# Kernel optimization log

Measured on AMD Instinct MI355X. Metric: run time of the kernel, lower is better.

The kernel has to match this reference:

```python
import jax, jax.numpy as jnp
import numpy as np

V, D, F, H, L = 32000, 1024, 4096, 16, 6
HD = D // H
EPS = 1e-5


def _posenc(S):
    pos = jnp.arange(S, dtype=jnp.float32)[:, None]
    div = jnp.exp(jnp.arange(0, D, 2, dtype=jnp.float32) * (-jnp.log(10000.0) / D))
    enc = jnp.zeros((S, D), jnp.float32)
    enc = enc.at[:, 0::2].set(jnp.sin(pos * div))
    enc = enc.at[:, 1::2].set(jnp.cos(pos * div))
    return enc


def _mha(xq, xkv, Wq, bq, Wk, bk, Wv, bv, Wo, bo, causal):
    B, Sq, _ = xq.shape
    Sk = xkv.shape[1]
    q = (xq @ Wq.T + bq).reshape(B, Sq, H, HD)
    k = (xkv @ Wk.T + bk).reshape(B, Sk, H, HD)
    v = (xkv @ Wv.T + bv).reshape(B, Sk, H, HD)
    scores = jnp.einsum('bqhd,bkhd->bhqk', q, k) / jnp.sqrt(jnp.float32(HD))
    if causal:
        mask = jnp.tril(jnp.ones((Sq, Sk), dtype=bool))
        scores = jnp.where(mask, scores, -jnp.inf)
    w = jax.nn.softmax(scores, axis=-1)
    out = jnp.einsum('bhqk,bkhd->bqhd', w, v).reshape(B, Sq, D)
    return out @ Wo.T + bo


def _ln(x, g, b):
    mu = jnp.mean(x, axis=-1, keepdims=True)
    var = jnp.mean((x - mu) ** 2, axis=-1, keepdims=True)
    return (x - mu) / jnp.sqrt(var + EPS) * g + b


def setup_inputs() -> dict:
    key = jax.random.key(0)
    ks = jax.random.split(key, 32)
    B, S, Se = 4, 512, 512
    s = 0.02
    inp = {
        'text': jax.random.randint(ks[0], (B, S), 0, V),
        'encoder_output': jax.random.normal(ks[1], (B, Se, D), jnp.float32),
        'W_e': jax.random.normal(ks[2], (V, D), jnp.float32) * s,
        'b_out': jnp.zeros((V,), jnp.float32),
        'ln_g': jnp.ones((D,), jnp.float32),
        'ln_b': jnp.zeros((D,), jnp.float32),
        'W1': jax.random.normal(ks[3], (F, D), jnp.float32) * s,
        'b1': jnp.zeros((F,), jnp.float32),
        'W2': jax.random.normal(ks[4], (D, F), jnp.float32) * s,
        'b2': jnp.zeros((D,), jnp.float32),
    }
    names = ['mWq', 'mWk', 'mWv', 'mWo', 'cWq', 'cWk', 'cWv', 'cWo']
    for i, n in enumerate(names):
        inp[n] = jax.random.normal(ks[5 + i], (D, D), jnp.float32) * s
        inp[n.replace('W', 'b')] = jnp.zeros((D,), jnp.float32)
    return inp


def reference(text, encoder_output, W_e, b_out, ln_g, ln_b, W1, b1, W2, b2,
              mWq, mbq, mWk, mbk, mWv, mbv, mWo, mbo,
              cWq, cbq, cWk, cbk, cWv, cbv, cWo, cbo):
    # embed + sinusoidal positional encoding (dropout is identity in eval)
    x = W_e[text] + _posenc(text.shape[1])[None, :, :]
    # NOTE: the torch module reuses the SAME attention/FFN/LN weights each layer
    for _ in range(L):
        a = _ln(x + _mha(x, x, mWq, mbq, mWk, mbk, mWv, mbv, mWo, mbo, True), ln_g, ln_b)
        c = _ln(_mha(a, encoder_output, cWq, cbq, cWk, cbk, cWv, cbv, cWo, cbo, False) + a, ln_g, ln_b)
        f = jax.nn.relu(c @ W1.T + b1) @ W2.T + b2
        x = _ln(c + f, ln_g, ln_b)
    logits = x @ W_e.T + b_out  # tied embedding weights
    # nn.Softmax() with dim=None on a 3-D tensor -> torch legacy dim=0
    return jax.nn.softmax(logits, axis=0)
```

## Files before the change

### kernel.cpp

```cpp
#include <hip/hip_runtime.h>

#define D_MODEL 1024
#define SEQ     512
#define NBATCH  4
#define NHEAD   16
#define HDIM    64
#define NTOK    2048
#define VOCAB   32000
#define FFDIM   4096
#define VCHUNK  6400
#define MiB     (1024*1024)

typedef _Float16 f16;
typedef f16   f16x8 __attribute__((ext_vector_type(8)));
typedef float f32x4 __attribute__((ext_vector_type(4)));

__device__ __forceinline__ void async_cp16(f16* lds, const f16* g) {
    __builtin_amdgcn_global_load_lds(
        (const __attribute__((address_space(1))) unsigned int*)g,
        (__attribute__((address_space(3))) unsigned int*)lds, 16, 0, 0);
}

__device__ __forceinline__ float block_sum(float v, float* lds) {
    #pragma unroll
    for (int o = 1; o < 64; o <<= 1) v += __shfl_xor(v, o);
    int w = threadIdx.x >> 6;
    if ((threadIdx.x & 63) == 0) lds[w] = v;
    __syncthreads();
    v = lds[0] + lds[1] + lds[2] + lds[3];
    __syncthreads();
    return v;
}
__device__ __forceinline__ float block_max(float v, float* lds) {
    #pragma unroll
    for (int o = 1; o < 64; o <<= 1) v = fmaxf(v, __shfl_xor(v, o));
    int w = threadIdx.x >> 6;
    if ((threadIdx.x & 63) == 0) lds[w] = v;
    __syncthreads();
    v = fmaxf(fmaxf(lds[0], lds[1]), fmaxf(lds[2], lds[3]));
    __syncthreads();
    return v;
}

__global__ __launch_bounds__(256) void f32_to_f16_kernel(
    const float* __restrict__ in, f16* __restrict__ out, int n)
{
    int i0 = blockIdx.x * 1024 + threadIdx.x;
    #pragma unroll
    for (int e = 0; e < 4; e++) {
        int i = i0 + e * 256;
        if (i < n) out[i] = (f16)in[i];
    }
}

__global__ __launch_bounds__(256) void embed_kernel(
    const int* __restrict__ text, const float* __restrict__ We,
    float* __restrict__ X, f16* __restrict__ X16)
{
    int t = blockIdx.x;
    int s = t & (SEQ - 1);
    int tok = text[t];
    int tid = threadIdx.x;
    const float kf = 9.210340371976184f / 1024.f;
    #pragma unroll
    for (int e = 0; e < 4; e++) {
        int d = tid + e * 256;
        int i2 = d & ~1;
        float freq = expf(-(float)i2 * kf);
        float ang = (float)s * freq;
        float pe = (d & 1) ? cosf(ang) : sinf(ang);
        float v = We[(size_t)tok * D_MODEL + d] + pe;
        X[(size_t)t * D_MODEL + d] = v;
        X16[(size_t)t * D_MODEL + d] = (f16)v;
    }
}

template<bool RELU, int OUTMODE, int BM, bool QKV3>
__global__ __launch_bounds__(256) void gemm16_kernel(
    const f16* __restrict__ A, const f16* __restrict__ W,
    const float* __restrict__ bias, const float* __restrict__ bias2,
    const float* __restrict__ bias3,
    float* __restrict__ C, f16* __restrict__ C16, int M, int N, int K)
{
    constexpr int AM = BM / 2;
    constexpr int TM = AM / 16;
    __shared__ __align__(16) f16 As[BM * 32];
    __shared__ __align__(16) f16 Bs[128 * 32];
    const int tid  = threadIdx.x;
    const int lane = tid & 63;
    const int wv   = tid >> 6;
    const int wr   = (wv >> 1) * AM;
    const int wc   = (wv & 1) * 64;
    const int m0 = blockIdx.y * BM;
    const int n0 = blockIdx.x * 128;
    const int lm = lane & 15;
    const int lk = (lane >> 4) * 8;

    f32x4 acc[TM][4] = {};

    for (int k0 = 0; k0 < K; k0 += 32) {
        #pragma unroll
        for (int e = 0; e < BM / 64; e++) {
            int s = tid + e * 256;
            int row = s >> 2, cb = s & 3;
            async_cp16(&As[s * 8], &A[(size_t)(m0 + row) * K + k0 + cb * 8]);
        }
        #pragma unroll
        for (int e = 0; e < 2; e++) {
            int s = tid + e * 256;
            int row = s >> 2, cb = s & 3;
            async_cp16(&Bs[s * 8], &W[(size_t)(n0 + row) * K + k0 + cb * 8]);
        }
        __syncthreads();
        f16x8 af[TM], bfr[4];
        #pragma unroll
        for (int i = 0; i < TM; i++)
            af[i]  = *(const f16x8*)&As[(wr + i * 16 + lm) * 32 + lk];
        #pragma unroll
        for (int j = 0; j < 4; j++)
            bfr[j] = *(const f16x8*)&Bs[(wc + j * 16 + lm) * 32 + lk];
        #pragma unroll
        for (int i = 0; i < TM; i++)
            #pragma unroll
            for (int j = 0; j < 4; j++)
                acc[i][j] = __builtin_amdgcn_mfma_f32_16x16x32_f16(
                    af[i], bfr[j], acc[i][j], 0, 0, 0);
        __syncthreads();
    }

    const int rq = (lane >> 4) * 4;
    #pragma unroll
    for (int i = 0; i < TM; i++) {
        #pragma unroll
        for (int j = 0; j < 4; j++) {
            int col = n0 + wc + j * 16 + lm;
            float bj;
            if (QKV3) {
                const float* bp = col < 1024 ? bias : (col < 2048 ? bias2 : bias3);
                bj = bp[col & 1023];
            } else {
                bj = bias[col];
            }
            #pragma unroll
            for (int r = 0; r < 4; r++) {
                int row = m0 + wr + i * 16 + rq + r;
                float v = acc[i][j][r] + bj;
                if (RELU) v = fmaxf(v, 0.f);
                if (OUTMODE == 0) C[(size_t)row * N + col] = v;
                else              C16[(size_t)row * N + col] = (f16)v;
            }
        }
    }
}

template<int CAUSAL>
__global__ __launch_bounds__(256) void attn_scores16_kernel(
    const f16* __restrict__ Qb, const f16* __restrict__ Kb,
    float* __restrict__ Sc, int ldq, int ldk, int qoff, int koff)
{
    const int bh = blockIdx.z;
    const int b = bh >> 4, h = bh & 15;
    const int q0 = blockIdx.y * 128, k0 = blockIdx.x * 128;
    const int tid = threadIdx.x;
    float* out = Sc + (size_t)bh * SEQ * SEQ;

    if (CAUSAL && k0 >= q0 + 128) {
        const f32x4 mv = {-1e30f, -1e30f, -1e30f, -1e30f};
        #pragma unroll
        for (int e = 0; e < 16; e++) {
            int idx = tid + e * 256;
            int rr = idx >> 5, c4 = (idx & 31) * 4;
            *(f32x4*)&out[(size_t)(q0 + rr) * SEQ + k0 + c4] = mv;
        }
        return;
    }

    __shared__ __align__(16) f16 As[128 * 64];
    __shared__ __align__(16) f16 Bs[128 * 64];
    const f16* Qg = Qb + (size_t)(b * SEQ + q0) * ldq + qoff + h * HDIM;
    const f16* Kg = Kb + (size_t)(b * SEQ + k0) * ldk + koff + h * HDIM;
    #pragma unroll
    for (int e = 0; e < 4; e++) {
        int s = tid + e * 256;
        int ks = s >> 9, row = (s >> 2) & 127, cb = s & 3;
        async_cp16(&As[s * 8], &Qg[(size_t)row * ldq + ks * 32 + cb * 8]);
        async_cp16(&Bs[s * 8], &Kg[(size_t)row * ldk + ks * 32 + cb * 8]);
    }
    __syncthreads();

    const int lane = tid & 63;
    const int wv   = tid >> 6;
    const int wr   = (wv >> 1) * 64;
    const int wc   = (wv & 1) * 64;
    const int lm   = lane & 15;
    const int lk   = (lane >> 4) * 8;
    f32x4 acc[4][4] = {};
    #pragma unroll
    for (int ks = 0; ks < 2; ks++) {
        f16x8 af[4], bf[4];
        #pragma unroll
        for (int i = 0; i < 4; i++)
            af[i] = *(const f16x8*)&As[ks * 4096 + (wr + i * 16 + lm) * 32 + lk];
        #pragma unroll
        for (int j = 0; j < 4; j++)
            bf[j] = *(const f16x8*)&Bs[ks * 4096 + (wc + j * 16 + lm) * 32 + lk];
        #pragma unroll
        for (int i = 0; i < 4; i++)
            #pragma unroll
            for (int j = 0; j < 4; j++)
                acc[i][j] = __builtin_amdgcn_mfma_f32_16x16x32_f16(
                    af[i], bf[j], acc[i][j], 0, 0, 0);
    }

    const int rq = (lane >> 4) * 4;
    #pragma unroll
    for (int i = 0; i < 4; i++)
        #pragma unroll
        for (int j = 0; j < 4; j++)
            #pragma unroll
            for (int r = 0; r < 4; r++) {
                int qq = q0 + wr + i * 16 + rq + r;
                int kk = k0 + wc + j * 16 + lm;
                float v = acc[i][j][r] * 0.125f;
                if (CAUSAL && kk > qq) v = -1e30f;
                out[(size_t)qq * SEQ + kk] = v;
            }
}

__global__ __launch_bounds__(256) void softmax_row_kernel(
    const float* __restrict__ Sc, f16* __restrict__ P)
{
    __shared__ float lds[4];
    size_t row = blockIdx.x;
    const float* p = Sc + row * SEQ;
    int tid = threadIdx.x;
    float v0 = p[tid], v1 = p[tid + 256];
    float m = block_max(fmaxf(v0, v1), lds);
    float e0 = expf(v0 - m), e1 = expf(v1 - m);
    float s = block_sum(e0 + e1, lds);
    float inv = 1.f / s;
    f16* q = P + row * SEQ;
    q[tid]       = (f16)(e0 * inv);
    q[tid + 256] = (f16)(e1 * inv);
}

__global__ __launch_bounds__(256) void attn_av16_kernel(
    const f16* __restrict__ P, const f16* __restrict__ Vt,
    f16* __restrict__ O16)
{
    __shared__ __align__(16) f16 Ps[64 * 32];
    __shared__ __align__(16) f16 Vs[64 * 32];
    const int bh = blockIdx.y;
    const int b = bh >> 4, h = bh & 15;
    const int q0 = blockIdx.x * 64;
    const int tid  = threadIdx.x;
    const int lane = tid & 63;
    const int wv   = tid >> 6;
    const int wr   = (wv >> 1) * 32;
    const int wc   = (wv & 1) * 32;
    const int lm   = lane & 15;
    const int lk   = (lane >> 4) * 8;
    const f16* Pg = P  + ((size_t)bh * SEQ + q0) * SEQ;
    const f16* Vg = Vt + (size_t)bh * HDIM * SEQ;

    f32x4 acc[2][2] = {};
    for (int k0 = 0; k0 < SEQ; k0 += 32) {
        int row = tid >> 2, cb = tid & 3;
        async_cp16(&Ps[tid * 8], &Pg[(size_t)row * SEQ + k0 + cb * 8]);
        async_cp16(&Vs[tid * 8], &Vg[(size_t)row * SEQ + k0 + cb * 8]);
        __syncthreads();
        f16x8 af[2], bf[2];
        #pragma unroll
        for (int i = 0; i < 2; i++)
            af[i] = *(const f16x8*)&Ps[(wr + i * 16 + lm) * 32 + lk];
        #pragma unroll
        for (int j = 0; j < 2; j++)
            bf[j] = *(const f16x8*)&Vs[(wc + j * 16 + lm) * 32 + lk];
        #pragma unroll
        for (int i = 0; i < 2; i++)
            #pragma unroll
            for (int j = 0; j < 2; j++)
                acc[i][j] = __builtin_amdgcn_mfma_f32_16x16x32_f16(
                    af[i], bf[j], acc[i][j], 0, 0, 0);
        __syncthreads();
    }

    const int rq = (lane >> 4) * 4;
    #pragma unroll
    for (int i = 0; i < 2; i++)
        #pragma unroll
        for (int j = 0; j < 2; j++)
            #pragma unroll
            for (int r = 0; r < 4; r++)
                O16[(size_t)(b * SEQ + q0 + wr + i * 16 + rq + r) * D_MODEL
                    + h * HDIM + wc + j * 16 + lm] = (f16)acc[i][j][r];
}

__global__ __launch_bounds__(256) void vtrans_kernel(
    const f16* __restrict__ V, f16* __restrict__ Vt, int ldv, int vbase)
{
    __shared__ __align__(16) f16 t[64][72];
    const int bh = blockIdx.y;
    const int b = bh >> 4, h = bh & 15;
    const int s0 = blockIdx.x * 64;
    const int tid = threadIdx.x;
    const int r = tid >> 3;
    const int c8 = (tid & 7) * 8;
    #pragma unroll
    for (int half = 0; half < 2; half++) {
        int row = r + half * 32;
        f16x8 v = *(const f16x8*)&V[(size_t)(b * SEQ + s0 + row) * ldv
                                    + vbase + h * HDIM + c8];
        #pragma unroll
        for (int j = 0; j < 8; j++) t[c8 + j][row] = v[j];
    }
    __syncthreads();
    const int d = tid >> 2;
    const int sblk = (tid & 3) * 16;
    f16* dst = Vt + ((size_t)bh * HDIM + d) * SEQ + s0 + sblk;
    *(f16x8*)&dst[0] = *(const f16x8*)&t[d][sblk];
    *(f16x8*)&dst[8] = *(const f16x8*)&t[d][sblk + 8];
}

__global__ __launch_bounds__(256) void add_ln_kernel(
    const float* __restrict__ X, const float* __restrict__ Y,
    const float* __restrict__ g, const float* __restrict__ bb,
    float* __restrict__ Out, f16* __restrict__ Out16)
{
    __shared__ float lds[4];
    int row = blockIdx.x;
    const float* xp = X + (size_t)row * D_MODEL;
    const float* yp = Y + (size_t)row * D_MODEL;
    int tid = threadIdx.x;
    float s[4];
    float lsum = 0.f;
    #pragma unroll
    for (int e = 0; e < 4; e++) {
        int d = tid + e * 256;
        s[e] = xp[d] + yp[d];
        lsum += s[e];
    }
    float mu = block_sum(lsum, lds) * (1.f / D_MODEL);
    float lv = 0.f;
    #pragma unroll
    for (int e = 0; e < 4; e++) { float t = s[e] - mu; lv += t * t; }
    float rstd = rsqrtf(block_sum(lv, lds) * (1.f / D_MODEL) + 1e-5f);
    #pragma unroll
    for (int e = 0; e < 4; e++) {
        int d = tid + e * 256;
        float v = (s[e] - mu) * rstd * g[d] + bb[d];
        Out[(size_t)row * D_MODEL + d] = v;
        Out16[(size_t)row * D_MODEL + d] = (f16)v;
    }
}

__global__ __launch_bounds__(256) void softmax_axis0_chunk_kernel(
    const float* __restrict__ L, float* __restrict__ out, int cv0)
{
    int idx = blockIdx.x * 256 + threadIdx.x;
    if (idx >= SEQ * VCHUNK) return;
    int s = idx / VCHUNK;
    int c = idx - s * VCHUNK;
    float v0 = L[((size_t)(0 * SEQ + s)) * VCHUNK + c];
    float v1 = L[((size_t)(1 * SEQ + s)) * VCHUNK + c];
    float v2 = L[((size_t)(2 * SEQ + s)) * VCHUNK + c];
    float v3 = L[((size_t)(3 * SEQ + s)) * VCHUNK + c];
    float m = fmaxf(fmaxf(v0, v1), fmaxf(v2, v3));
    float e0 = expf(v0 - m), e1 = expf(v1 - m), e2 = expf(v2 - m), e3 = expf(v3 - m);
    float inv = 1.f / (e0 + e1 + e2 + e3);
    out[((size_t)(0 * SEQ + s)) * VOCAB + cv0 + c] = e0 * inv;
    out[((size_t)(1 * SEQ + s)) * VOCAB + cv0 + c] = e1 * inv;
    out[((size_t)(2 * SEQ + s)) * VOCAB + cv0 + c] = e2 * inv;
    out[((size_t)(3 * SEQ + s)) * VOCAB + cv0 + c] = e3 * inv;
}

extern "C" void kernel_launch(void* const* d_in, const int* in_sizes, int n_in,
                              void* d_out, int out_size, void* d_ws, size_t ws_size,
                              hipStream_t stream)
{
    const int*   text = (const int*)d_in[0];
    const float* enc  = (const float*)d_in[1];
    const float* W_e  = (const float*)d_in[2];
    const float* b_out= (const float*)d_in[3];
    const float* ln_g = (const float*)d_in[4];
    const float* ln_b = (const float*)d_in[5];
    const float* W1   = (const float*)d_in[6];
    const float* b1   = (const float*)d_in[7];
    const float* W2   = (const float*)d_in[8];
    const float* b2   = (const float*)d_in[9];
    const float* mWq  = (const float*)d_in[10]; const float* mbq = (const float*)d_in[11];
    const float* mWk  = (const float*)d_in[12]; const float* mbk = (const float*)d_in[13];
    const float* mWv  = (const float*)d_in[14]; const float* mbv = (const float*)d_in[15];
    const float* mWo  = (const float*)d_in[16]; const float* mbo = (const float*)d_in[17];
    const float* cWq  = (const float*)d_in[18]; const float* cbq = (const float*)d_in[19];
    const float* cWk  = (const float*)d_in[20]; const float* cbk = (const float*)d_in[21];
    const float* cWv  = (const float*)d_in[22]; const float* cbv = (const float*)d_in[23];
    const float* cWo  = (const float*)d_in[24]; const float* cbo = (const float*)d_in[25];
    float* out = (float*)d_out;

    char* w8 = (char*)d_ws;
    float* x    = (float*)(w8 +   0 * (size_t)MiB);
    float* a    = (float*)(w8 +   8 * (size_t)MiB);
    float* c    = (float*)(w8 +  16 * (size_t)MiB);
    float* Sc   = (float*)(w8 +  24 * (size_t)MiB);
    float* o    = (float*)(w8 +  80 * (size_t)MiB);
    float* logits = Sc;
    char* scratch = w8 + 88 * (size_t)MiB;
    f16* P16    = (f16*)scratch;
    f16* ffh16  = (f16*)scratch;
    f16* cWk16s = (f16*)scratch;
    f16* cWv16s = (f16*)(scratch + 2 * (size_t)MiB);
    f16* enc16  = (f16*)(scratch + 4 * (size_t)MiB);
    f16* qkv16  = (f16*)(w8 + 120 * (size_t)MiB);
    f16* q16    = qkv16;
    f16* vt16   = (f16*)(w8 + 132 * (size_t)MiB);
    f16* enck16 = (f16*)(w8 + 136 * (size_t)MiB);
    f16* encvt16= (f16*)(w8 + 140 * (size_t)MiB);
    f16* attn16 = (f16*)(w8 + 144 * (size_t)MiB);
    f16* x16    = (f16*)(w8 + 148 * (size_t)MiB);
    f16* a16    = (f16*)(w8 + 152 * (size_t)MiB);
    f16* c16    = (f16*)(w8 + 156 * (size_t)MiB);
    f16* mQKV16 = (f16*)(w8 + 160 * (size_t)MiB);
    f16* mWo16  = (f16*)(w8 + 166 * (size_t)MiB);
    f16* cWq16  = (f16*)(w8 + 168 * (size_t)MiB);
    f16* cWo16  = (f16*)(w8 + 170 * (size_t)MiB);
    f16* W116   = (f16*)(w8 + 172 * (size_t)MiB);
    f16* W216   = (f16*)(w8 + 180 * (size_t)MiB);
    f16* We16   = (f16*)(w8 + 188 * (size_t)MiB);

    auto conv = [&](const float* src, f16* dst, int n) {
        f32_to_f16_kernel<<<(n + 1023) / 1024, 256, 0, stream>>>(src, dst, n);
    };

    const int DD = D_MODEL * D_MODEL;
    conv(mWq, mQKV16, DD);
    conv(mWk, mQKV16 + (size_t)DD, DD);
    conv(mWv, mQKV16 + 2 * (size_t)DD, DD);
    conv(mWo, mWo16, DD);
    conv(cWq, cWq16, DD); conv(cWk, cWk16s, DD); conv(cWv, cWv16s, DD); conv(cWo, cWo16, DD);
    conv(W1, W116, FFDIM * D_MODEL); conv(W2, W216, FFDIM * D_MODEL);
    conv(W_e, We16, VOCAB * D_MODEL);
    conv(enc, enc16, NTOK * D_MODEL);

    embed_kernel<<<NTOK, 256, 0, stream>>>(text, W_e, x, x16);

    gemm16_kernel<false, 1, 64, false><<<dim3(D_MODEL / 128, NTOK / 64), 256, 0, stream>>>(
        enc16, cWk16s, cbk, nullptr, nullptr, nullptr, enck16, NTOK, D_MODEL, D_MODEL);
    gemm16_kernel<false, 1, 64, false><<<dim3(D_MODEL / 128, NTOK / 64), 256, 0, stream>>>(
        enc16, cWv16s, cbv, nullptr, nullptr, nullptr, attn16, NTOK, D_MODEL, D_MODEL);
    vtrans_kernel<<<dim3(SEQ / 64, NBATCH * NHEAD), 256, 0, stream>>>(
        attn16, encvt16, D_MODEL, 0);

    const int BH = NBATCH * NHEAD;
    for (int layer = 0; layer < 6; layer++) {
        gemm16_kernel<false, 1, 64, true><<<dim3(3072 / 128, NTOK / 64), 256, 0, stream>>>(
            x16, mQKV16, mbq, mbk, mbv, nullptr, qkv16, NTOK, 3072, D_MODEL);
        vtrans_kernel<<<dim3(SEQ / 64, BH), 256, 0, stream>>>(qkv16, vt16, 3072, 2048);
        attn_scores16_kernel<1><<<dim3(SEQ / 128, SEQ / 128, BH), 256, 0, stream>>>(
            qkv16, qkv16, Sc, 3072, 3072, 0, 1024);
        softmax_row_kernel<<<BH * SEQ, 256, 0, stream>>>(Sc, P16);
        attn_av16_kernel<<<dim3(SEQ / 64, BH), 256, 0, stream>>>(P16, vt16, attn16);
        gemm16_kernel<false, 0, 64, false><<<dim3(D_MODEL / 128, NTOK / 64), 256, 0, stream>>>(
            attn16, mWo16, mbo, nullptr, nullptr, o, nullptr, NTOK, D_MODEL, D_MODEL);
        add_ln_kernel<<<NTOK, 256, 0, stream>>>(x, o, ln_g, ln_b, a, a16);

        gemm16_kernel<false, 1, 64, false><<<dim3(D_MODEL / 128, NTOK / 64), 256, 0, stream>>>(
            a16, cWq16, cbq, nullptr, nullptr, nullptr, q16, NTOK, D_MODEL, D_MODEL);
        attn_scores16_kernel<0><<<dim3(SEQ / 128, SEQ / 128, BH), 256, 0, stream>>>(
            q16, enck16, Sc, D_MODEL, D_MODEL, 0, 0);
        softmax_row_kernel<<<BH * SEQ, 256, 0, stream>>>(Sc, P16);
        attn_av16_kernel<<<dim3(SEQ / 64, BH), 256, 0, stream>>>(P16, encvt16, attn16);
        gemm16_kernel<false, 0, 64, false><<<dim3(D_MODEL / 128, NTOK / 64), 256, 0, stream>>>(
            attn16, cWo16, cbo, nullptr, nullptr, o, nullptr, NTOK, D_MODEL, D_MODEL);
        add_ln_kernel<<<NTOK, 256, 0, stream>>>(o, a, ln_g, ln_b, c, c16);

        gemm16_kernel<true, 1, 128, false><<<dim3(FFDIM / 128, NTOK / 128), 256, 0, stream>>>(
            c16, W116, b1, nullptr, nullptr, nullptr, ffh16, NTOK, FFDIM, D_MODEL);
        gemm16_kernel<false, 0, 64, false><<<dim3(D_MODEL / 128, NTOK / 64), 256, 0, stream>>>(
            ffh16, W216, b2, nullptr, nullptr, o, nullptr, NTOK, D_MODEL, FFDIM);
        add_ln_kernel<<<NTOK, 256, 0, stream>>>(c, o, ln_g, ln_b, x, x16);
    }

    for (int ch = 0; ch < VOCAB / VCHUNK; ch++) {
        int cv0 = ch * VCHUNK;
        gemm16_kernel<false, 0, 128, false><<<dim3(VCHUNK / 128, NTOK / 128), 256, 0, stream>>>(
            x16, We16 + (size_t)cv0 * D_MODEL, b_out + cv0, nullptr, nullptr,
            logits, nullptr, NTOK, VCHUNK, D_MODEL);
        softmax_axis0_chunk_kernel<<<(SEQ * VCHUNK + 255) / 256, 256, 0, stream>>>(
            logits, out, cv0);
    }
}
```

Baseline: 2.777 ms.

## Fuse attention scores with softmax, skip masked causal work, fuse output softmax into GEMM

Attention scores and the row softmax are fused into one kernel that keeps scores in registers with double-buffered K tiles, so the fp32 score matrix is no longer written and reread. Causal blocks skip fully masked key tiles in both the score and AV kernels. The last layer-norm writes its f16 output interleaved by batch, so each group of four accumulator rows in the vocab GEMM holds the four batch entries of one position and the axis-0 softmax runs in the GEMM epilogue. This removes the logits buffer and the chunked softmax pass. The embed kernel now handles all batches per position. Register pressure from 32 accumulator tiles per wave and strided output stores are the trade-off.

```diff
diff --git a/kernel.cpp b/kernel.cpp
--- a/kernel.cpp
+++ b/kernel.cpp
@@ -8,7 +8,6 @@
 #define NTOK    2048
 #define VOCAB   32000
 #define FFDIM   4096
-#define VCHUNK  6400
 #define MiB     (1024*1024)
 
 typedef _Float16 f16;
@@ -31,16 +30,6 @@
     __syncthreads();
     return v;
 }
-__device__ __forceinline__ float block_max(float v, float* lds) {
-    #pragma unroll
-    for (int o = 1; o < 64; o <<= 1) v = fmaxf(v, __shfl_xor(v, o));
-    int w = threadIdx.x >> 6;
-    if ((threadIdx.x & 63) == 0) lds[w] = v;
-    __syncthreads();
-    v = fmaxf(fmaxf(lds[0], lds[1]), fmaxf(lds[2], lds[3]));
-    __syncthreads();
-    return v;
-}
 
 __global__ __launch_bounds__(256) void f32_to_f16_kernel(
     const float* __restrict__ in, f16* __restrict__ out, int n)
@@ -57,10 +46,11 @@
     const int* __restrict__ text, const float* __restrict__ We,
     float* __restrict__ X, f16* __restrict__ X16)
 {
-    int t = blockIdx.x;
-    int s = t & (SEQ - 1);
-    int tok = text[t];
+    int s = blockIdx.x;
     int tid = threadIdx.x;
+    int tok[NBATCH];
+    #pragma unroll
+    for (int b = 0; b < NBATCH; b++) tok[b] = text[b * SEQ + s];
     const float kf = 9.210340371976184f / 1024.f;
     #pragma unroll
     for (int e = 0; e < 4; e++) {
@@ -69,9 +59,13 @@
         float freq = expf(-(float)i2 * kf);
         float ang = (float)s * freq;
         float pe = (d & 1) ? cosf(ang) : sinf(ang);
-        float v = We[(size_t)tok * D_MODEL + d] + pe;
-        X[(size_t)t * D_MODEL + d] = v;
-        X16[(size_t)t * D_MODEL + d] = (f16)v;
+        #pragma unroll
+        for (int b = 0; b < NBATCH; b++) {
+            float v = We[(size_t)tok[b] * D_MODEL + d] + pe;
+            size_t off = (size_t)(b * SEQ + s) * D_MODEL + d;
+            X[off] = v;
+            X16[off] = (f16)v;
+        }
     }
 }
 
@@ -141,112 +135,147 @@
             } else {
                 bj = bias[col];
             }
-            #pragma unroll
-            for (int r = 0; r < 4; r++) {
-                int row = m0 + wr + i * 16 + rq + r;
-                float v = acc[i][j][r] + bj;
-                if (RELU) v = fmaxf(v, 0.f);
-                if (OUTMODE == 0) C[(size_t)row * N + col] = v;
-                else              C16[(size_t)row * N + col] = (f16)v;
+            if (OUTMODE == 2) {
+                int srow = (m0 + wr + i * 16 + rq) >> 2;
+                float v[4];
+                float mx = -1e30f;
+                #pragma unroll
+                for (int r = 0; r < 4; r++) {
+                    v[r] = acc[i][j][r] + bj;
+                    mx = fmaxf(mx, v[r]);
+                }
+                float ssum = 0.f;
+                #pragma unroll
+                for (int r = 0; r < 4; r++) { v[r] = expf(v[r] - mx); ssum += v[r]; }
+                float inv = 1.f / ssum;
+                #pragma unroll
+                for (int r = 0; r < 4; r++)
+                    C[((size_t)r * SEQ + srow) * N + col] = v[r] * inv;
+            } else {
+                #pragma unroll
+                for (int r = 0; r < 4; r++) {
+                    int row = m0 + wr + i * 16 + rq + r;
+                    float v = acc[i][j][r] + bj;
+                    if (RELU) v = fmaxf(v, 0.f);
+                    if (OUTMODE == 0) C[(size_t)row * N + col] = v;
+                    else              C16[(size_t)row * N + col] = (f16)v;
+                }
             }
         }
     }
 }
 
 template<int CAUSAL>
-__global__ __launch_bounds__(256) void attn_scores16_kernel(
+__global__ __launch_bounds__(256) void attn_sm_kernel(
     const f16* __restrict__ Qb, const f16* __restrict__ Kb,
-    float* __restrict__ Sc, int ldq, int ldk, int qoff, int koff)
-{
-    const int bh = blockIdx.z;
+    f16* __restrict__ P, int ldq, int ldk, int qoff, int koff)
+{
+    __shared__ __align__(16) f16 Qs[2][64][32];
+    __shared__ __align__(16) f16 Ks[2][2][128][32];
+    const int bh = blockIdx.y;
     const int b = bh >> 4, h = bh & 15;
-    const int q0 = blockIdx.y * 128, k0 = blockIdx.x * 128;
-    const int tid = threadIdx.x;
-    float* out = Sc + (size_t)bh * SEQ * SEQ;
-
-    if (CAUSAL && k0 >= q0 + 128) {
-        const f32x4 mv = {-1e30f, -1e30f, -1e30f, -1e30f};
-        #pragma unroll
-        for (int e = 0; e < 16; e++) {
-            int idx = tid + e * 256;
-            int rr = idx >> 5, c4 = (idx & 31) * 4;
-            *(f32x4*)&out[(size_t)(q0 + rr) * SEQ + k0 + c4] = mv;
-        }
-        return;
-    }
-
-    __shared__ __align__(16) f16 As[128 * 64];
-    __shared__ __align__(16) f16 Bs[128 * 64];
-    const f16* Qg = Qb + (size_t)(b * SEQ + q0) * ldq + qoff + h * HDIM;
-    const f16* Kg = Kb + (size_t)(b * SEQ + k0) * ldk + koff + h * HDIM;
-    #pragma unroll
-    for (int e = 0; e < 4; e++) {
-        int s = tid + e * 256;
-        int ks = s >> 9, row = (s >> 2) & 127, cb = s & 3;
-        async_cp16(&As[s * 8], &Qg[(size_t)row * ldq + ks * 32 + cb * 8]);
-        async_cp16(&Bs[s * 8], &Kg[(size_t)row * ldk + ks * 32 + cb * 8]);
-    }
-    __syncthreads();
-
+    const int q0 = blockIdx.x * 64;
+    const int tid  = threadIdx.x;
     const int lane = tid & 63;
-    const int wv   = tid >> 6;
-    const int wr   = (wv >> 1) * 64;
-    const int wc   = (wv & 1) * 64;
+    const int w    = tid >> 6;
     const int lm   = lane & 15;
     const int lk   = (lane >> 4) * 8;
-    f32x4 acc[4][4] = {};
-    #pragma unroll
-    for (int ks = 0; ks < 2; ks++) {
-        f16x8 af[4], bf[4];
-        #pragma unroll
-        for (int i = 0; i < 4; i++)
-            af[i] = *(const f16x8*)&As[ks * 4096 + (wr + i * 16 + lm) * 32 + lk];
-        #pragma unroll
-        for (int j = 0; j < 4; j++)
-            bf[j] = *(const f16x8*)&Bs[ks * 4096 + (wc + j * 16 + lm) * 32 + lk];
-        #pragma unroll
-        for (int i = 0; i < 4; i++)
+    const int nkt  = CAUSAL ? (q0 >> 7) + 1 : 4;
+    const int nj   = nkt * 8;
+
+    const f16* Qg = Qb + (size_t)(b * SEQ + q0) * ldq + qoff + h * HDIM;
+    const f16* Kg = Kb + (size_t)(b * SEQ) * ldk + koff + h * HDIM;
+
+    #pragma unroll
+    for (int e = 0; e < 2; e++) {
+        int cc = tid + e * 256;
+        int ks = cc >> 8, row = (cc >> 2) & 63, cb = cc & 3;
+        async_cp16(&Qs[ks][row][cb * 8], &Qg[(size_t)row * ldq + ks * 32 + cb * 8]);
+    }
+    #pragma unroll
+    for (int e = 0; e < 4; e++) {
+        int cc = tid + e * 256;
+        int ks = cc >> 9, row = (cc >> 2) & 127, cb = cc & 3;
+        async_cp16(&Ks[0][ks][row][cb * 8], &Kg[(size_t)row * ldk + ks * 32 + cb * 8]);
+    }
+    __syncthreads();
+
+    f16x8 af[2];
+    af[0] = *(const f16x8*)&Qs[0][w * 16 + lm][lk];
+    af[1] = *(const f16x8*)&Qs[1][w * 16 + lm][lk];
+
+    f32x4 acc[32] = {};
+
+    #pragma unroll
+    for (int kt = 0; kt < 4; kt++) {
+        if (kt < nkt) {
+            if (kt + 1 < nkt) {
+                const f16* src = Kg + (size_t)(kt + 1) * 128 * ldk;
+                int buf = (kt + 1) & 1;
+                #pragma unroll
+                for (int e = 0; e < 4; e++) {
+                    int cc = tid + e * 256;
+                    int ks = cc >> 9, row = (cc >> 2) & 127, cb = cc & 3;
+                    async_cp16(&Ks[buf][ks][row][cb * 8],
+                               &src[(size_t)row * ldk + ks * 32 + cb * 8]);
+                }
+            }
             #pragma unroll
-            for (int j = 0; j < 4; j++)
-                acc[i][j] = __builtin_amdgcn_mfma_f32_16x16x32_f16(
-                    af[i], bf[j], acc[i][j], 0, 0, 0);
+            for (int ks = 0; ks < 2; ks++)
+                #pragma unroll
+                for (int j = 0; j < 8; j++) {
+                    f16x8 bf = *(const f16x8*)&Ks[kt & 1][ks][j * 16 + lm][lk];
+                    acc[kt * 8 + j] = __builtin_amdgcn_mfma_f32_16x16x32_f16(
+                        af[ks], bf, acc[kt * 8 + j], 0, 0, 0);
+                }
+            if (kt + 1 < nkt) __syncthreads();
+        }
     }
 
     const int rq = (lane >> 4) * 4;
     #pragma unroll
-    for (int i = 0; i < 4; i++)
-        #pragma unroll
-        for (int j = 0; j < 4; j++)
-            #pragma unroll
-            for (int r = 0; r < 4; r++) {
-                int qq = q0 + wr + i * 16 + rq + r;
-                int kk = k0 + wc + j * 16 + lm;
-                float v = acc[i][j][r] * 0.125f;
-                if (CAUSAL && kk > qq) v = -1e30f;
-                out[(size_t)qq * SEQ + kk] = v;
+    for (int r = 0; r < 4; r++) {
+        const int qq = q0 + w * 16 + rq + r;
+        float mr = -1e30f;
+        #pragma unroll
+        for (int j = 0; j < 32; j++) {
+            if (j < nj) {
+                float v = acc[j][r] * 0.125f;
+                if (CAUSAL && (j * 16 + lm) > qq) v = -1e30f;
+                acc[j][r] = v;
+                mr = fmaxf(mr, v);
             }
-}
-
-__global__ __launch_bounds__(256) void softmax_row_kernel(
-    const float* __restrict__ Sc, f16* __restrict__ P)
-{
-    __shared__ float lds[4];
-    size_t row = blockIdx.x;
-    const float* p = Sc + row * SEQ;
-    int tid = threadIdx.x;
-    float v0 = p[tid], v1 = p[tid + 256];
-    float m = block_max(fmaxf(v0, v1), lds);
-    float e0 = expf(v0 - m), e1 = expf(v1 - m);
-    float s = block_sum(e0 + e1, lds);
-    float inv = 1.f / s;
-    f16* q = P + row * SEQ;
-    q[tid]       = (f16)(e0 * inv);
-    q[tid + 256] = (f16)(e1 * inv);
+        }
+        mr = fmaxf(mr, __shfl_xor(mr, 1));
+        mr = fmaxf(mr, __shfl_xor(mr, 2));
+        mr = fmaxf(mr, __shfl_xor(mr, 4));
+        mr = fmaxf(mr, __shfl_xor(mr, 8));
+        float sum = 0.f;
+        #pragma unroll
+        for (int j = 0; j < 32; j++) {
+            if (j < nj) {
+                float e = expf(acc[j][r] - mr);
+                acc[j][r] = e;
+                sum += e;
+            }
+        }
+        sum += __shfl_xor(sum, 1);
+        sum += __shfl_xor(sum, 2);
+        sum += __shfl_xor(sum, 4);
+        sum += __shfl_xor(sum, 8);
+        float inv = 1.f / sum;
+        f16* prow = P + ((size_t)bh * SEQ + qq) * SEQ + lm;
+        #pragma unroll
+        for (int j = 0; j < 32; j++) {
+            float pv = (j < nj) ? acc[j][r] * inv : 0.f;
+            prow[j * 16] = (f16)pv;
+        }
+    }
 }
 
 __global__ __launch_bounds__(256) void attn_av16_kernel(
     const f16* __restrict__ P, const f16* __restrict__ Vt,
-    f16* __restrict__ O16)
+    f16* __restrict__ O16, int causal)
 {
     __shared__ __align__(16) f16 Ps[64 * 32];
     __shared__ __align__(16) f16 Vs[64 * 32];
@@ -262,9 +291,10 @@
     const int lk   = (lane >> 4) * 8;
     const f16* Pg = P  + ((size_t)bh * SEQ + q0) * SEQ;
     const f16* Vg = Vt + (size_t)bh * HDIM * SEQ;
+    const int klim = causal ? q0 + 64 : SEQ;
 
     f32x4 acc[2][2] = {};
-    for (int k0 = 0; k0 < SEQ; k0 += 32) {
+    for (int k0 = 0; k0 < klim; k0 += 32) {
         int row = tid >> 2, cb = tid & 3;
         async_cp16(&Ps[tid * 8], &Pg[(size_t)row * SEQ + k0 + cb * 8]);
         async_cp16(&Vs[tid * 8], &Vg[(size_t)row * SEQ + k0 + cb * 8]);
@@ -322,6 +352,7 @@
     *(f16x8*)&dst[8] = *(const f16x8*)&t[d][sblk + 8];
 }
 
+template<bool IL>
 __global__ __launch_bounds__(256) void add_ln_kernel(
     const float* __restrict__ X, const float* __restrict__ Y,
     const float* __restrict__ g, const float* __restrict__ bb,
@@ -345,33 +376,14 @@
     #pragma unroll
     for (int e = 0; e < 4; e++) { float t = s[e] - mu; lv += t * t; }
     float rstd = rsqrtf(block_sum(lv, lds) * (1.f / D_MODEL) + 1e-5f);
+    int orow = IL ? ((row & (SEQ - 1)) * 4 + (row >> 9)) : row;
     #pragma unroll
     for (int e = 0; e < 4; e++) {
         int d = tid + e * 256;
         float v = (s[e] - mu) * rstd * g[d] + bb[d];
         Out[(size_t)row * D_MODEL + d] = v;
-        Out16[(size_t)row * D_MODEL + d] = (f16)v;
-    }
-}
-
-__global__ __launch_bounds__(256) void softmax_axis0_chunk_kernel(
-    const float* __restrict__ L, float* __restrict__ out, int cv0)
-{
-    int idx = blockIdx.x * 256 + threadIdx.x;
-    if (idx >= SEQ * VCHUNK) return;
-    int s = idx / VCHUNK;
-    int c = idx - s * VCHUNK;
-    float v0 = L[((size_t)(0 * SEQ + s)) * VCHUNK + c];
-    float v1 = L[((size_t)(1 * SEQ + s)) * VCHUNK + c];
-    float v2 = L[((size_t)(2 * SEQ + s)) * VCHUNK + c];
-    float v3 = L[((size_t)(3 * SEQ + s)) * VCHUNK + c];
-    float m = fmaxf(fmaxf(v0, v1), fmaxf(v2, v3));
-    float e0 = expf(v0 - m), e1 = expf(v1 - m), e2 = expf(v2 - m), e3 = expf(v3 - m);
-    float inv = 1.f / (e0 + e1 + e2 + e3);
-    out[((size_t)(0 * SEQ + s)) * VOCAB + cv0 + c] = e0 * inv;
-    out[((size_t)(1 * SEQ + s)) * VOCAB + cv0 + c] = e1 * inv;
-    out[((size_t)(2 * SEQ + s)) * VOCAB + cv0 + c] = e2 * inv;
-    out[((size_t)(3 * SEQ + s)) * VOCAB + cv0 + c] = e3 * inv;
+        Out16[(size_t)orow * D_MODEL + d] = (f16)v;
+    }
 }
 
 extern "C" void kernel_launch(void* const* d_in, const int* in_sizes, int n_in,
@@ -402,9 +414,7 @@
     float* x    = (float*)(w8 +   0 * (size_t)MiB);
     float* a    = (float*)(w8 +   8 * (size_t)MiB);
     float* c    = (float*)(w8 +  16 * (size_t)MiB);
-    float* Sc   = (float*)(w8 +  24 * (size_t)MiB);
     float* o    = (float*)(w8 +  80 * (size_t)MiB);
-    float* logits = Sc;
     char* scratch = w8 + 88 * (size_t)MiB;
     f16* P16    = (f16*)scratch;
     f16* ffh16  = (f16*)scratch;
@@ -442,7 +452,7 @@
     conv(W_e, We16, VOCAB * D_MODEL);
     conv(enc, enc16, NTOK * D_MODEL);
 
-    embed_kernel<<<NTOK, 256, 0, stream>>>(text, W_e, x, x16);
+    embed_kernel<<<SEQ, 256, 0, stream>>>(text, W_e, x, x16);
 
     gemm16_kernel<false, 1, 64, false><<<dim3(D_MODEL / 128, NTOK / 64), 256, 0, stream>>>(
         enc16, cWk16s, cbk, nullptr, nullptr, nullptr, enck16, NTOK, D_MODEL, D_MODEL);
@@ -456,37 +466,32 @@
         gemm16_kernel<false, 1, 64, true><<<dim3(3072 / 128, NTOK / 64), 256, 0, stream>>>(
             x16, mQKV16, mbq, mbk, mbv, nullptr, qkv16, NTOK, 3072, D_MODEL);
         vtrans_kernel<<<dim3(SEQ / 64, BH), 256, 0, stream>>>(qkv16, vt16, 3072, 2048);
-        attn_scores16_kernel<1><<<dim3(SEQ / 128, SEQ / 128, BH), 256, 0, stream>>>(
-            qkv16, qkv16, Sc, 3072, 3072, 0, 1024);
-        softmax_row_kernel<<<BH * SEQ, 256, 0, stream>>>(Sc, P16);
-        attn_av16_kernel<<<dim3(SEQ / 64, BH), 256, 0, stream>>>(P16, vt16, attn16);
+        attn_sm_kernel<1><<<dim3(SEQ / 64, BH), 256, 0, stream>>>(
+            qkv16, qkv16, P16, 3072, 3072, 0, 1024);
+        attn_av16_kernel<<<dim3(SEQ / 64, BH), 256, 0, stream>>>(P16, vt16, attn16, 1);
         gemm16_kernel<false, 0, 64, false><<<dim3(D_MODEL / 128, NTOK / 64), 256, 0, stream>>>(
             attn16, mWo16, mbo, nullptr, nullptr, o, nullptr, NTOK, D_MODEL, D_MODEL);
-        add_ln_kernel<<<NTOK, 256, 0, stream>>>(x, o, ln_g, ln_b, a, a16);
+        add_ln_kernel<false><<<NTOK, 256, 0, stream>>>(x, o, ln_g, ln_b, a, a16);
 
         gemm16_kernel<false, 1, 64, false><<<dim3(D_MODEL / 128, NTOK / 64), 256, 0, stream>>>(
             a16, cWq16, cbq, nullptr, nullptr, nullptr, q16, NTOK, D_MODEL, D_MODEL);
-        attn_scores16_kernel<0><<<dim3(SEQ / 128, SEQ / 128, BH), 256, 0, stream>>>(
-            q16, enck16, Sc, D_MODEL, D_MODEL, 0, 0);
-        softmax_row_kernel<<<BH * SEQ, 256, 0, stream>>>(Sc, P16);
-        attn_av16_kernel<<<dim3(SEQ / 64, BH), 256, 0, stream>>>(P16, encvt16, attn16);
+        attn_sm_kernel<0><<<dim3(SEQ / 64, BH), 256, 0, stream>>>(
+            q16, enck16, P16, D_MODEL, D_MODEL, 0, 0);
+        attn_av16_kernel<<<dim3(SEQ / 64, BH), 256, 0, stream>>>(P16, encvt16, attn16, 0);
         gemm16_kernel<false, 0, 64, false><<<dim3(D_MODEL / 128, NTOK / 64), 256, 0, stream>>>(
             attn16, cWo16, cbo, nullptr, nullptr, o, nullptr, NTOK, D_MODEL, D_MODEL);
-        add_ln_kernel<<<NTOK, 256, 0, stream>>>(o, a, ln_g, ln_b, c, c16);
+        add_ln_kernel<false><<<NTOK, 256, 0, stream>>>(o, a, ln_g, ln_b, c, c16);
 
         gemm16_kernel<true, 1, 128, false><<<dim3(FFDIM / 128, NTOK / 128), 256, 0, stream>>>(
             c16, W116, b1, nullptr, nullptr, nullptr, ffh16, NTOK, FFDIM, D_MODEL);
         gemm16_kernel<false, 0, 64, false><<<dim3(D_MODEL / 128, NTOK / 64), 256, 0, stream>>>(
             ffh16, W216, b2, nullptr, nullptr, o, nullptr, NTOK, D_MODEL, FFDIM);
-        add_ln_kernel<<<NTOK, 256, 0, stream>>>(c, o, ln_g, ln_b, x, x16);
-    }
-
-    for (int ch = 0; ch < VOCAB / VCHUNK; ch++) {
-        int cv0 = ch * VCHUNK;
-        gemm16_kernel<false, 0, 128, false><<<dim3(VCHUNK / 128, NTOK / 128), 256, 0, stream>>>(
-            x16, We16 + (size_t)cv0 * D_MODEL, b_out + cv0, nullptr, nullptr,
-            logits, nullptr, NTOK, VCHUNK, D_MODEL);
-        softmax_axis0_chunk_kernel<<<(SEQ * VCHUNK + 255) / 256, 256, 0, stream>>>(
-            logits, out, cv0);
-    }
-}
+        if (layer < 5)
+            add_ln_kernel<false><<<NTOK, 256, 0, stream>>>(c, o, ln_g, ln_b, x, x16);
+        else
+            add_ln_kernel<true><<<NTOK, 256, 0, stream>>>(c, o, ln_g, ln_b, x, x16);
+    }
+
+    gemm16_kernel<false, 2, 128, false><<<dim3(VOCAB / 128, NTOK / 128), 256, 0, stream>>>(
+        x16, We16, b_out, nullptr, nullptr, out, nullptr, NTOK, VOCAB, D_MODEL);
+}
```

New measurement: 2.445 ms. 11.9% less time.
